# Kernel optimization log

Hardware: AMD Instinct MI355X
Metric: run time of the kernel (lower is better)

The kernel has to match this reference:

```python
import jax, jax.numpy as jnp
import numpy as np
import math

HEADS = 8
HID = 32
MODES = 8
IN_CH = 4
SEQ = 32
B = 2
H = 64
W = 64


def spectral_conv(x, wr, wi):
    # x: [N, Cin, H, W]; w: [Cin, Cout, m, m] complex (low rfft2 modes only)
    n, _, h, w = x.shape
    m = wr.shape[2]
    xf = jnp.fft.rfft2(x)  # [N, Cin, H, W//2+1] complex64
    of = jnp.einsum('bixy,ioxy->boxy', xf[:, :, :m, :m], wr + 1j * wi)
    out_ft = jnp.zeros((n, wr.shape[1], h, w // 2 + 1), dtype=of.dtype)
    out_ft = out_ft.at[:, :, :m, :m].set(of)
    return jnp.fft.irfft2(out_ft, s=(h, w))


def conv1x1(x, w, b):
    # x: [N, Cin, H, W], w: [Cout, Cin], b: [Cout]
    return jnp.einsum('bchw,oc->bohw', x, w) + b[None, :, None, None]


def setup_inputs() -> dict:
    key = jax.random.key(0)
    ks = jax.random.split(key, 16)
    hd = HEADS * HID
    s = 0.02
    inp = {
        'v': jax.random.normal(ks[0], (B, SEQ, IN_CH, H, W), dtype=jnp.float32),
        'qwr': jax.random.normal(ks[1], (IN_CH, hd, MODES, MODES), dtype=jnp.float32) * s,
        'qwi': jax.random.normal(ks[2], (IN_CH, hd, MODES, MODES), dtype=jnp.float32) * s,
        'kwr': jax.random.normal(ks[3], (IN_CH, hd, MODES, MODES), dtype=jnp.float32) * s,
        'kwi': jax.random.normal(ks[4], (IN_CH, hd, MODES, MODES), dtype=jnp.float32) * s,
        'vwr': jax.random.normal(ks[5], (IN_CH, hd, MODES, MODES), dtype=jnp.float32) * s,
        'vwi': jax.random.normal(ks[6], (IN_CH, hd, MODES, MODES), dtype=jnp.float32) * s,
        'u1wr': jax.random.normal(ks[7], (hd, HID, MODES, MODES), dtype=jnp.float32) * s,
        'u1wi': jax.random.normal(ks[8], (hd, HID, MODES, MODES), dtype=jnp.float32) * s,
        'u2wr': jax.random.normal(ks[9], (HID, IN_CH, MODES, MODES), dtype=jnp.float32) * s,
        'u2wi': jax.random.normal(ks[10], (HID, IN_CH, MODES, MODES), dtype=jnp.float32) * s,
        's1w': jax.random.normal(ks[11], (HID, hd), dtype=jnp.float32) * s,
        's1b': jnp.zeros((HID,), dtype=jnp.float32),
        's2w': jax.random.normal(ks[12], (IN_CH, HID), dtype=jnp.float32) * s,
        's2b': jnp.zeros((IN_CH,), dtype=jnp.float32),
    }
    return inp


def reference(v, qwr, qwi, kwr, kwi, vwr, vwi, u1wr, u1wi, u2wr, u2wi, s1w, s1b, s2w, s2b):
    b, s, c, h, w = v.shape
    scale = 1.0 / math.sqrt(HID / HEADS)
    vr = v.reshape(b * s, c, h, w)
    embed = (b, HEADS, s, -1, h, w)  # same raw row-major reshape as torch
    q = spectral_conv(vr, qwr, qwi).reshape(embed)
    k = spectral_conv(vr, kwr, kwi).reshape(embed)
    val = spectral_conv(vr, vwr, vwi).reshape(embed)
    # inner products over channel dim, then dx^2-weighted spatial integral
    ip = jnp.einsum('bhsdrc,bhtdrc->bhstrc', q, k) * scale
    dx = 1.0 / h
    l2 = jnp.sum(ip, axis=(-2, -1)) * (dx * dx)  # [b, h, s1, s2]
    A = jax.nn.softmax(l2, axis=-1)
    u = jnp.einsum('bhst,bhtdrc->bhsdrc', A, val)
    u = jnp.transpose(u, (0, 2, 1, 3, 4, 5)).reshape(b * s, HEADS * u.shape[3], h, w)
    # SimpleFNO: gelu(conv1) + skip1, then conv2 + skip2
    x1 = jax.nn.gelu(spectral_conv(u, u1wr, u1wi), approximate=False) + conv1x1(u, s1w, s1b)
    x2 = spectral_conv(x1, u2wr, u2wi) + conv1x1(x1, s2w, s2b)
    return x2.reshape(b, s, c, h, w)
```

## Files before the change

kernel.cpp:

```cpp
#include <hip/hip_runtime.h>
#include <math.h>

#define HEADS 8
#define HIDC  32
#define MODES 8
#define IN_CH 4
#define SEQ   32
#define NS    64
#define HD    256
#define NM    64
#define NPIX  4096
#define TWO_PI_D 6.283185307179586476925286766559

__device__ __forceinline__ float2 f2(float a, float b){ return make_float2(a,b); }

__global__ __launch_bounds__(256) void fwd_dft_kernel(const float* __restrict__ src,
                                                      float2* __restrict__ dst){
  int f = blockIdx.x;
  const float* fld = src + (size_t)f * NPIX;
  __shared__ float  s_fld[64*65];
  __shared__ float2 s_cs[64];
  __shared__ float2 s_a1[64][8];
  int tid = threadIdx.x;
  for (int k = tid; k < NPIX; k += 256) s_fld[(k>>6)*65 + (k&63)] = fld[k];
  if (tid < 64){ double sv, cv; sincos(TWO_PI_D * tid / 64.0, &sv, &cv); s_cs[tid] = f2((float)cv,(float)sv); }
  __syncthreads();
  for (int o = tid; o < 512; o += 256){
    int y = o >> 3, kx = o & 7;
    const float* row = s_fld + y*65;
    float sr = 0.f, si = 0.f;
    for (int x = 0; x < 64; ++x){
      float2 cs = s_cs[(kx*x) & 63];
      float v = row[x];
      sr += v * cs.x; si -= v * cs.y;
    }
    s_a1[y][kx] = f2(sr, si);
  }
  __syncthreads();
  if (tid < 64){
    int ky = tid >> 3, kx = tid & 7;
    float sr = 0.f, si = 0.f;
    for (int y = 0; y < 64; ++y){
      float2 a = s_a1[y][kx];
      float2 cs = s_cs[(ky*y) & 63];
      sr += a.x*cs.x + a.y*cs.y;
      si += a.y*cs.x - a.x*cs.y;
    }
    dst[(size_t)f*NM + tid] = f2(sr, si);
  }
}

__global__ __launch_bounds__(256) void gram_kernel(const float* __restrict__ qwr, const float* __restrict__ qwi,
                                                   const float* __restrict__ kwr, const float* __restrict__ kwi,
                                                   float2* __restrict__ G2, float* __restrict__ Gdc){
  int m = blockIdx.x, tid = threadIdx.x;
  __shared__ float qsr[4][257], qsi[4][257], ksr[4][257], ksi[4][257];
  for (int k = tid; k < 1024; k += 256){
    int i = k >> 8, c = k & 255;
    size_t a = ((size_t)(i*256 + c))*64 + m;
    qsr[i][c] = qwr[a]; qsi[i][c] = qwi[a];
    ksr[i][c] = kwr[a]; ksi[i][c] = kwi[a];
  }
  __syncthreads();
  int kx = m & 7, ky = m >> 3;
  float w = (kx >= 1) ? 2.0f : ((ky >= 1) ? 0.5f : 0.0f);
  for (int e = tid; e < 1024; e += 256){
    int P = e >> 7, T = (e >> 4) & 7, i = (e >> 2) & 3, j = e & 3;
    float grr=0.f, gri=0.f, gir=0.f, gii=0.f;
    for (int d = 0; d < 32; ++d){
      float ar = qsr[i][P*32+d], ai = qsi[i][P*32+d];
      float br = ksr[j][T*32+d], bi = ksi[j][T*32+d];
      grr += ar*br; gri += ar*bi; gir += ai*br; gii += ai*bi;
    }
    G2[(size_t)(((m*8+P)*4+i)*4+j)*8 + T] = f2(w*(grr+gii), w*(gir-gri));
    if (m == 0){
      int o = ((P*4+i)*4+j)*8 + T;
      Gdc[o] = grr; Gdc[1024+o] = gri; Gdc[2048+o] = gir; Gdc[3072+o] = gii;
    }
  }
}

__global__ __launch_bounds__(256) void attn_kernel(const float2* __restrict__ Vf,
                                                   const float2* __restrict__ G2,
                                                   const float* __restrict__ Gdc,
                                                   float* __restrict__ A){
  int bx = blockIdx.x;
  int s = bx & 31;
  int base = ((bx >> 8) * 32) + (((bx >> 5) & 7) * 4);
  int tid = threadIdx.x;
  int t = tid & 31, mc = tid >> 5;
  __shared__ float2 s_vf[4][IN_CH][64];
  __shared__ float  s_part[8][33];
  for (int k = tid; k < 4*IN_CH*64; k += 256){
    int m = k & 63, c = (k>>6)&3, smp = k>>8;
    s_vf[smp][c][m] = Vf[((size_t)(base+smp)*IN_CH + c)*NM + m];
  }
  __syncthreads();
  int sg = s >> 3, P = s & 7;
  int tg = t >> 3, T = t & 7;
  float acc = 0.f;
  for (int mm = 0; mm < 8; ++mm){
    int m = mc*8 + mm;
    const float2* g = G2 + (size_t)((m*8+P)*16)*8 + T;
    float sub = 0.f;
    for (int i = 0; i < 4; ++i){
      float2 a = s_vf[sg][i][m];
      for (int j = 0; j < 4; ++j){
        float2 b = s_vf[tg][j][m];
        float zr = a.x*b.x + a.y*b.y;
        float zi = a.y*b.x - a.x*b.y;
        float2 gv = g[(size_t)(i*4+j)*8];
        sub += zr*gv.x - zi*gv.y;
      }
    }
    acc += sub;
  }
  if (mc == 0){
    float sub = 0.f;
    for (int i = 0; i < 4; ++i){
      float2 a = s_vf[sg][i][0];
      for (int j = 0; j < 4; ++j){
        float2 b = s_vf[tg][j][0];
        int o = ((P*4+i)*4+j)*8 + T;
        sub += a.x*b.x*Gdc[o] - a.x*b.y*Gdc[1024+o]
             - a.y*b.x*Gdc[2048+o] + a.y*b.y*Gdc[3072+o];
      }
    }
    acc += sub;
  }
  s_part[mc][t] = acc;
  __syncthreads();
  if (tid < 32){
    float l2 = 0.f;
    for (int k = 0; k < 8; ++k) l2 += s_part[k][tid];
    l2 *= 0.5f / (4096.0f * 4096.0f);
    float mx = l2;
    for (int off = 16; off; off >>= 1) mx = fmaxf(mx, __shfl_xor(mx, off, 32));
    float e = expf(l2 - mx);
    float sm = e;
    for (int off = 16; off; off >>= 1) sm += __shfl_xor(sm, off, 32);
    A[(size_t)bx*32 + tid] = e / sm;
  }
}

__global__ __launch_bounds__(256) void uspec_kernel(const float2* __restrict__ Vf,
                                                    const float* __restrict__ vwr, const float* __restrict__ vwi,
                                                    const float* __restrict__ A,
                                                    float2* __restrict__ Uf){
  int bid = blockIdx.x;
  int b = bid >> 7, hh = (bid >> 4) & 7, mq = bid & 15, m0 = mq*4;
  int nbase = b*32 + hh*4;
  int tid = threadIdx.x;
  __shared__ float2 s_vw[4][4][256];
  __shared__ float2 s_vv[4][4][256];
  __shared__ float  s_A[32][32];
  __shared__ float2 s_vf[4][4][4];
  for (int k = tid; k < 4096; k += 256){
    int i = k >> 10, c = (k >> 2) & 255, mm = k & 3;
    size_t a = ((size_t)(i*256 + c))*64 + m0 + mm;
    s_vw[i][mm][c] = f2(vwr[a], vwi[a]);
  }
  for (int k = tid; k < 1024; k += 256)
    s_A[k>>5][k&31] = A[(size_t)((b*8+hh)*32 + (k>>5))*32 + (k&31)];
  if (tid < 64){
    int smp = tid >> 4, i = (tid >> 2) & 3, mm = tid & 3;
    s_vf[smp][i][mm] = Vf[((size_t)(nbase+smp)*4 + i)*64 + m0 + mm];
  }
  __syncthreads();
  for (int k = tid; k < 4096; k += 256){
    int smp = k >> 10, mm = (k >> 8) & 3, c = k & 255;
    float sr = 0.f, si = 0.f;
    for (int i = 0; i < 4; ++i){
      float2 v = s_vf[smp][i][mm];
      float2 w = s_vw[i][mm][c];
      sr += v.x*w.x - v.y*w.y;
      si += v.x*w.y + v.y*w.x;
    }
    s_vv[smp][mm][c] = f2(sr, si);
  }
  __syncthreads();
  int sg = tid >> 5, d = tid & 31;
  float2 acc[4][4];
  for (int ss = 0; ss < 4; ++ss)
    for (int mm = 0; mm < 4; ++mm) acc[ss][mm] = f2(0.f, 0.f);
  for (int tt = 0; tt < 32; ++tt){
    int tg = tt >> 3, c = (tt & 7)*32 + d;
    float a0 = s_A[sg*4+0][tt], a1 = s_A[sg*4+1][tt];
    float a2 = s_A[sg*4+2][tt], a3 = s_A[sg*4+3][tt];
    for (int mm = 0; mm < 4; ++mm){
      float2 v = s_vv[tg][mm][c];
      acc[0][mm].x += a0*v.x; acc[0][mm].y += a0*v.y;
      acc[1][mm].x += a1*v.x; acc[1][mm].y += a1*v.y;
      acc[2][mm].x += a2*v.x; acc[2][mm].y += a2*v.y;
      acc[3][mm].x += a3*v.x; acc[3][mm].y += a3*v.y;
    }
  }
  for (int ss = 0; ss < 4; ++ss){
    int n = b*32 + sg*4 + ss;
    for (int mm = 0; mm < 4; ++mm)
      Uf[((size_t)n*64 + m0 + mm)*256 + hh*32 + d] = acc[ss][mm];
  }
}

__global__ __launch_bounds__(256) void mix1_kernel(const float2* __restrict__ Uf,
                                                   const float* __restrict__ u1wr, const float* __restrict__ u1wi,
                                                   const float* __restrict__ s1w,
                                                   float2* __restrict__ U1f, float2* __restrict__ S1f){
  int n = blockIdx.x >> 2, mq = blockIdx.x & 3, m0 = mq*16;
  int tid = threadIdx.x;
  __shared__ float2 s_u[16][258];
  __shared__ float  s_w1[32][257];
  for (int k = tid; k < 16*256; k += 256){
    int c = k & 255, mm = k >> 8;
    s_u[mm][c] = Uf[((size_t)n*64 + m0 + mm)*256 + c];
  }
  for (int k = tid; k < 32*256; k += 256){
    int c = k & 255, o1 = k >> 8;
    s_w1[o1][c] = s1w[o1*256 + c];
  }
  __syncthreads();
  int o1 = tid >> 3, m8 = tid & 7;
  int mA = m0 + m8, mB = m0 + m8 + 8;
  float prA = ((mA & 7)==0 && mA) ? 0.5f : 1.0f;  float piA = mA ? prA : 0.0f;
  float prB = ((mB & 7)==0 && mB) ? 0.5f : 1.0f;  float piB = mB ? prB : 0.0f;
  float2 au0 = f2(0,0), au1 = f2(0,0), as0 = f2(0,0), as1 = f2(0,0);
  for (int c = 0; c < 256; ++c){
    float2 uA = s_u[m8][c], uB = s_u[m8+8][c];
    float sw = s_w1[o1][c];
    size_t wb = ((size_t)c*32 + o1)*64;
    float wrA = u1wr[wb + mA], wiA = u1wi[wb + mA];
    float wrB = u1wr[wb + mB], wiB = u1wi[wb + mB];
    float xA = uA.x*prA, yA = uA.y*piA;
    float xB = uB.x*prB, yB = uB.y*piB;
    au0.x += xA*wrA - yA*wiA;  au0.y += xA*wiA + yA*wrA;
    au1.x += xB*wrB - yB*wiB;  au1.y += xB*wiB + yB*wrB;
    as0.x += uA.x*sw; as0.y += uA.y*sw;
    as1.x += uB.x*sw; as1.y += uB.y*sw;
  }
  size_t ob = (size_t)(n*32 + o1)*64;
  U1f[ob + mA] = au0; U1f[ob + mB] = au1;
  S1f[ob + mA] = as0; S1f[ob + mB] = as1;
}

__global__ __launch_bounds__(256) void x1dft_kernel(const float2* __restrict__ U1f,
                                                    const float2* __restrict__ S1f,
                                                    const float* __restrict__ s1b,
                                                    float* __restrict__ x1,
                                                    float2* __restrict__ X1f){
  int f = blockIdx.x, o1 = f & 31, tid = threadIdx.x;
  __shared__ float2 s_cs[64];
  __shared__ float2 s_gu[64], s_gs[64];
  __shared__ float2 s_tu[64][8], s_ts[64][8];
  __shared__ float  s_fld[64*65];
  __shared__ float2 s_a1[64][8];
  if (tid < 64){ double sv, cv; sincos(TWO_PI_D*tid/64.0, &sv, &cv); s_cs[tid] = f2((float)cv,(float)sv); }
  else if (tid < 128) s_gu[tid-64]  = U1f[(size_t)f*NM + tid-64];
  else if (tid < 192) s_gs[tid-128] = S1f[(size_t)f*NM + tid-128];
  __syncthreads();
  for (int o = tid; o < 512; o += 256){
    int y = o >> 3, kx = o & 7;
    float wf = (kx ? 2.0f : 1.0f) * (1.0f/4096.0f);
    float ar=0.f, ai=0.f, br=0.f, bi=0.f;
    for (int ky = 0; ky < 8; ++ky){
      float2 cs = s_cs[(ky*y) & 63];
      float2 gu = s_gu[ky*8+kx], gs = s_gs[ky*8+kx];
      ar += gu.x*cs.x - gu.y*cs.y;  ai += gu.x*cs.y + gu.y*cs.x;
      br += gs.x*cs.x - gs.y*cs.y;  bi += gs.x*cs.y + gs.y*cs.x;
    }
    s_tu[y][kx] = f2(ar*wf, ai*wf);
    s_ts[y][kx] = f2(br*wf, bi*wf);
  }
  __syncthreads();
  float bias = s1b[o1];
  float* dst = x1 + (size_t)f*NPIX;
  for (int p = tid; p < NPIX; p += 256){
    int y = p >> 6, x = p & 63;
    float vu = 0.f, vs = 0.f;
    for (int kx = 0; kx < 8; ++kx){
      float2 cs = s_cs[(kx*x) & 63];
      float2 tu = s_tu[y][kx], ts = s_ts[y][kx];
      vu += tu.x*cs.x - tu.y*cs.y;
      vs += ts.x*cs.x - ts.y*cs.y;
    }
    float g = 0.5f * vu * (1.0f + erff(vu * 0.70710678f));
    float val = g + vs + bias;
    dst[p] = val;
    s_fld[y*65 + x] = val;
  }
  __syncthreads();
  for (int o = tid; o < 512; o += 256){
    int y = o >> 3, kx = o & 7;
    const float* row = s_fld + y*65;
    float sr = 0.f, si = 0.f;
    for (int x = 0; x < 64; ++x){
      float2 cs = s_cs[(kx*x) & 63];
      float v = row[x];
      sr += v*cs.x; si -= v*cs.y;
    }
    s_a1[y][kx] = f2(sr, si);
  }
  __syncthreads();
  if (tid < 64){
    int ky = tid >> 3, kx = tid & 7;
    float sr = 0.f, si = 0.f;
    for (int y = 0; y < 64; ++y){
      float2 a = s_a1[y][kx];
      float2 cs = s_cs[(ky*y) & 63];
      sr += a.x*cs.x + a.y*cs.y;
      si += a.y*cs.x - a.x*cs.y;
    }
    X1f[(size_t)f*NM + tid] = f2(sr, si);
  }
}

__global__ __launch_bounds__(256) void final_kernel(const float2* __restrict__ X1f,
                                                    const float* __restrict__ u2wr, const float* __restrict__ u2wi,
                                                    const float* __restrict__ x1,
                                                    const float* __restrict__ s2w, const float* __restrict__ s2b,
                                                    float* __restrict__ out){
  int n = blockIdx.x >> 3, tile = blockIdx.x & 7;
  int tid = threadIdx.x;
  __shared__ float2 s_cs[64];
  __shared__ float2 s_x2f[4][64];
  __shared__ float2 s_tmp[4][64][8];
  __shared__ float  s_w2[128];
  __shared__ float  s_b2[4];
  if (tid < 64){ double sv, cv; sincos(TWO_PI_D*tid/64.0, &sv, &cv); s_cs[tid] = f2((float)cv,(float)sv); }
  if (tid >= 64 && tid < 192) s_w2[tid-64] = s2w[tid-64];
  if (tid >= 192 && tid < 196) s_b2[tid-192] = s2b[tid-192];
  {
    int o2 = tid >> 6, m = tid & 63;
    float sr = 0.f, si = 0.f;
    for (int o1 = 0; o1 < 32; ++o1){
      float2 xv = X1f[((size_t)n*HIDC + o1)*NM + m];
      size_t wb = ((size_t)(o1*IN_CH + o2))*NM + m;
      float wr = u2wr[wb], wi = u2wi[wb];
      sr += xv.x*wr - xv.y*wi;
      si += xv.x*wi + xv.y*wr;
    }
    s_x2f[o2][m] = f2(sr, si);
  }
  __syncthreads();
  for (int o = tid; o < 2048; o += 256){
    int o2 = o >> 9, rem = o & 511, y = rem >> 3, kx = rem & 7;
    float wf = (kx ? 2.0f : 1.0f) * (1.0f/4096.0f);
    float tr=0.f, ti=0.f;
    for (int ky = 0; ky < 8; ++ky){
      float2 cs = s_cs[(ky*y) & 63];
      float2 g = s_x2f[o2][ky*8+kx];
      tr += g.x*cs.x - g.y*cs.y;
      ti += g.x*cs.y + g.y*cs.x;
    }
    s_tmp[o2][y][kx] = f2(tr*wf, ti*wf);
  }
  __syncthreads();
  const float* xbase = x1 + (size_t)n*HIDC*NPIX;
  float* obase = out + (size_t)n*IN_CH*NPIX;
  for (int p = tile*512 + tid; p < (tile+1)*512; p += 256){
    float a0 = s_b2[0], a1 = s_b2[1], a2 = s_b2[2], a3 = s_b2[3];
    for (int c = 0; c < 32; ++c){
      float xv = xbase[(size_t)c*NPIX + p];
      a0 += s_w2[c]*xv; a1 += s_w2[32+c]*xv; a2 += s_w2[64+c]*xv; a3 += s_w2[96+c]*xv;
    }
    int y = p >> 6, x = p & 63;
    float sp[4];
    #pragma unroll
    for (int o2 = 0; o2 < 4; ++o2){
      float v = 0.f;
      for (int kx = 0; kx < 8; ++kx){
        float2 cs = s_cs[(kx*x) & 63];
        float2 t2 = s_tmp[o2][y][kx];
        v += t2.x*cs.x - t2.y*cs.y;
      }
      sp[o2] = v;
    }
    obase[p]          = a0 + sp[0];
    obase[NPIX + p]   = a1 + sp[1];
    obase[2*NPIX + p] = a2 + sp[2];
    obase[3*NPIX + p] = a3 + sp[3];
  }
}

extern "C" void kernel_launch(void* const* d_in, const int* in_sizes, int n_in,
                              void* d_out, int out_size, void* d_ws, size_t ws_size,
                              hipStream_t stream) {
  (void)in_sizes; (void)n_in; (void)out_size; (void)ws_size;
  const float* v    = (const float*)d_in[0];
  const float* qwr  = (const float*)d_in[1];
  const float* qwi  = (const float*)d_in[2];
  const float* kwr  = (const float*)d_in[3];
  const float* kwi  = (const float*)d_in[4];
  const float* vwr  = (const float*)d_in[5];
  const float* vwi  = (const float*)d_in[6];
  const float* u1wr = (const float*)d_in[7];
  const float* u1wi = (const float*)d_in[8];
  const float* u2wr = (const float*)d_in[9];
  const float* u2wi = (const float*)d_in[10];
  const float* s1w  = (const float*)d_in[11];
  const float* s1b  = (const float*)d_in[12];
  const float* s2w  = (const float*)d_in[13];
  const float* s2b  = (const float*)d_in[14];
  float* out = (float*)d_out;

  float* ws = (float*)d_ws;
  size_t off = 0;
  float2* Vf   = (float2*)(ws + off); off += (size_t)NS*IN_CH*NM*2;
  float2* G2   = (float2*)(ws + off); off += (size_t)65536*2;
  float*  Gdc  =          (ws + off); off += 4096;
  float*  A    =          (ws + off); off += 16384;
  float2* Uf   = (float2*)(ws + off); off += (size_t)NS*NM*HD*2;
  float2* U1f  = (float2*)(ws + off); off += (size_t)NS*HIDC*NM*2;
  float2* S1f  = (float2*)(ws + off); off += (size_t)NS*HIDC*NM*2;
  float*  x1   =          (ws + off); off += (size_t)NS*HIDC*NPIX;
  float2* X1f  = (float2*)(ws + off); off += (size_t)NS*HIDC*NM*2;

  fwd_dft_kernel<<<NS*IN_CH, 256, 0, stream>>>(v, Vf);
  gram_kernel<<<64, 256, 0, stream>>>(qwr, qwi, kwr, kwi, G2, Gdc);
  attn_kernel<<<512, 256, 0, stream>>>(Vf, G2, Gdc, A);
  uspec_kernel<<<256, 256, 0, stream>>>(Vf, vwr, vwi, A, Uf);
  mix1_kernel<<<256, 256, 0, stream>>>(Uf, u1wr, u1wi, s1w, U1f, S1f);
  x1dft_kernel<<<NS*HIDC, 256, 0, stream>>>(U1f, S1f, s1b, x1, X1f);
  final_kernel<<<64*8, 256, 0, stream>>>(X1f, u2wr, u2wi, x1, s2w, s2b, out);
}
```

Measured before the change: 224.0 us.

## Pre-transpose u1 weights, split uspec/mix1/final finer, tabulate DFT twiddles

Adds a kernel that transposes and pre-scales the u1 spectral weights into a float4 layout, so mix1 can read them coalesced with one thread per output and mode. uspec, mix1 and final are split into more, smaller blocks to raise parallelism. x1dft and final use a precomputed 64x8 twiddle table with float4 shared-memory reads and register-cached column twiddles in place of indexed cos/sin lookups. The transposed weights are stored in the x1 buffer, which x1dft overwrites later. The cost is an extra launch and redundant per-block work such as repeated twiddle and weight setup.

```diff
diff --git a/kernel.cpp b/kernel.cpp
--- a/kernel.cpp
+++ b/kernel.cpp
@@ -148,27 +148,28 @@
                                                     const float* __restrict__ A,
                                                     float2* __restrict__ Uf){
   int bid = blockIdx.x;
-  int b = bid >> 7, hh = (bid >> 4) & 7, mq = bid & 15, m0 = mq*4;
+  int mg = bid & 31, hh = (bid >> 5) & 7, b = bid >> 8;
+  int m0 = mg*2;
   int nbase = b*32 + hh*4;
   int tid = threadIdx.x;
-  __shared__ float2 s_vw[4][4][256];
-  __shared__ float2 s_vv[4][4][256];
-  __shared__ float  s_A[32][32];
-  __shared__ float2 s_vf[4][4][4];
-  for (int k = tid; k < 4096; k += 256){
-    int i = k >> 10, c = (k >> 2) & 255, mm = k & 3;
-    size_t a = ((size_t)(i*256 + c))*64 + m0 + mm;
+  __shared__ float2 s_vw[4][2][256];
+  __shared__ float2 s_vv[4][2][256];
+  __shared__ float  s_A[32][33];
+  __shared__ float2 s_vf[4][4][2];
+  for (int k = tid; k < 2048; k += 256){
+    int i = k >> 9, mm = (k >> 8) & 1, c = k & 255;
+    size_t a = ((size_t)i*256 + c)*64 + m0 + mm;
     s_vw[i][mm][c] = f2(vwr[a], vwi[a]);
   }
   for (int k = tid; k < 1024; k += 256)
     s_A[k>>5][k&31] = A[(size_t)((b*8+hh)*32 + (k>>5))*32 + (k&31)];
-  if (tid < 64){
-    int smp = tid >> 4, i = (tid >> 2) & 3, mm = tid & 3;
+  if (tid < 32){
+    int smp = tid >> 3, i = (tid >> 1) & 3, mm = tid & 1;
     s_vf[smp][i][mm] = Vf[((size_t)(nbase+smp)*4 + i)*64 + m0 + mm];
   }
   __syncthreads();
-  for (int k = tid; k < 4096; k += 256){
-    int smp = k >> 10, mm = (k >> 8) & 3, c = k & 255;
+  for (int k = tid; k < 2048; k += 256){
+    int smp = k >> 9, mm = (k >> 8) & 1, c = k & 255;
     float sr = 0.f, si = 0.f;
     for (int i = 0; i < 4; ++i){
       float2 v = s_vf[smp][i][mm];
@@ -180,14 +181,14 @@
   }
   __syncthreads();
   int sg = tid >> 5, d = tid & 31;
-  float2 acc[4][4];
+  float2 acc[4][2];
   for (int ss = 0; ss < 4; ++ss)
-    for (int mm = 0; mm < 4; ++mm) acc[ss][mm] = f2(0.f, 0.f);
+    for (int mm = 0; mm < 2; ++mm) acc[ss][mm] = f2(0.f, 0.f);
   for (int tt = 0; tt < 32; ++tt){
     int tg = tt >> 3, c = (tt & 7)*32 + d;
     float a0 = s_A[sg*4+0][tt], a1 = s_A[sg*4+1][tt];
     float a2 = s_A[sg*4+2][tt], a3 = s_A[sg*4+3][tt];
-    for (int mm = 0; mm < 4; ++mm){
+    for (int mm = 0; mm < 2; ++mm){
       float2 v = s_vv[tg][mm][c];
       acc[0][mm].x += a0*v.x; acc[0][mm].y += a0*v.y;
       acc[1][mm].x += a1*v.x; acc[1][mm].y += a1*v.y;
@@ -197,49 +198,52 @@
   }
   for (int ss = 0; ss < 4; ++ss){
     int n = b*32 + sg*4 + ss;
-    for (int mm = 0; mm < 4; ++mm)
+    for (int mm = 0; mm < 2; ++mm)
       Uf[((size_t)n*64 + m0 + mm)*256 + hh*32 + d] = acc[ss][mm];
   }
 }
 
-__global__ __launch_bounds__(256) void mix1_kernel(const float2* __restrict__ Uf,
-                                                   const float* __restrict__ u1wr, const float* __restrict__ u1wi,
+__global__ __launch_bounds__(256) void u1t_kernel(const float* __restrict__ u1wr,
+                                                  const float* __restrict__ u1wi,
+                                                  float4* __restrict__ u1wT){
+  int t = blockIdx.x*256 + threadIdx.x;
+  int o1 = t & 31, c = (t>>5) & 255, m = t >> 13;
+  float pr = ((m & 7)==0 && m) ? 0.5f : 1.0f;
+  float pi = m ? pr : 0.0f;
+  size_t src = ((size_t)c*32 + o1)*64 + m;
+  float wr = u1wr[src], wi = u1wi[src];
+  u1wT[t] = make_float4(pr*wr, pi*wi, pr*wi, pi*wr);
+}
+
+__global__ __launch_bounds__(128) void mix1_kernel(const float2* __restrict__ Uf,
+                                                   const float4* __restrict__ u1wT,
                                                    const float* __restrict__ s1w,
                                                    float2* __restrict__ U1f, float2* __restrict__ S1f){
-  int n = blockIdx.x >> 2, mq = blockIdx.x & 3, m0 = mq*16;
+  int n = blockIdx.x >> 4, mg = blockIdx.x & 15, m0 = mg*4;
   int tid = threadIdx.x;
-  __shared__ float2 s_u[16][258];
-  __shared__ float  s_w1[32][257];
-  for (int k = tid; k < 16*256; k += 256){
-    int c = k & 255, mm = k >> 8;
+  __shared__ float2 s_u[4][256];
+  for (int k = tid; k < 1024; k += 128){
+    int mm = k >> 8, c = k & 255;
     s_u[mm][c] = Uf[((size_t)n*64 + m0 + mm)*256 + c];
   }
-  for (int k = tid; k < 32*256; k += 256){
-    int c = k & 255, o1 = k >> 8;
-    s_w1[o1][c] = s1w[o1*256 + c];
-  }
-  __syncthreads();
-  int o1 = tid >> 3, m8 = tid & 7;
-  int mA = m0 + m8, mB = m0 + m8 + 8;
-  float prA = ((mA & 7)==0 && mA) ? 0.5f : 1.0f;  float piA = mA ? prA : 0.0f;
-  float prB = ((mB & 7)==0 && mB) ? 0.5f : 1.0f;  float piB = mB ? prB : 0.0f;
-  float2 au0 = f2(0,0), au1 = f2(0,0), as0 = f2(0,0), as1 = f2(0,0);
+  __syncthreads();
+  int o1 = tid & 31, mm = tid >> 5;
+  int m = m0 + mm;
+  const float4* wp = u1wT + (size_t)m*256*32 + o1;
+  const float* swp = s1w + o1*256;
+  float2 au = f2(0.f,0.f), asv = f2(0.f,0.f);
+  #pragma unroll 8
   for (int c = 0; c < 256; ++c){
-    float2 uA = s_u[m8][c], uB = s_u[m8+8][c];
-    float sw = s_w1[o1][c];
-    size_t wb = ((size_t)c*32 + o1)*64;
-    float wrA = u1wr[wb + mA], wiA = u1wi[wb + mA];
-    float wrB = u1wr[wb + mB], wiB = u1wi[wb + mB];
-    float xA = uA.x*prA, yA = uA.y*piA;
-    float xB = uB.x*prB, yB = uB.y*piB;
-    au0.x += xA*wrA - yA*wiA;  au0.y += xA*wiA + yA*wrA;
-    au1.x += xB*wrB - yB*wiB;  au1.y += xB*wiB + yB*wrB;
-    as0.x += uA.x*sw; as0.y += uA.y*sw;
-    as1.x += uB.x*sw; as1.y += uB.y*sw;
-  }
-  size_t ob = (size_t)(n*32 + o1)*64;
-  U1f[ob + mA] = au0; U1f[ob + mB] = au1;
-  S1f[ob + mA] = as0; S1f[ob + mB] = as1;
+    float2 u = s_u[mm][c];
+    float4 w = wp[(size_t)c*32];
+    float sw = swp[c];
+    au.x  += u.x*w.x - u.y*w.y;
+    au.y  += u.x*w.z + u.y*w.w;
+    asv.x += u.x*sw;
+    asv.y += u.y*sw;
+  }
+  size_t ob = ((size_t)n*32 + o1)*64 + m;
+  U1f[ob] = au; S1f[ob] = asv;
 }
 
 __global__ __launch_bounds__(256) void x1dft_kernel(const float2* __restrict__ U1f,
@@ -248,21 +252,25 @@
                                                     float* __restrict__ x1,
                                                     float2* __restrict__ X1f){
   int f = blockIdx.x, o1 = f & 31, tid = threadIdx.x;
-  __shared__ float2 s_cs[64];
+  __shared__ float2 s_e[64][8];
   __shared__ float2 s_gu[64], s_gs[64];
   __shared__ float2 s_tu[64][8], s_ts[64][8];
-  __shared__ float  s_fld[64*65];
+  __shared__ float  s_fld[64*68];
   __shared__ float2 s_a1[64][8];
-  if (tid < 64){ double sv, cv; sincos(TWO_PI_D*tid/64.0, &sv, &cv); s_cs[tid] = f2((float)cv,(float)sv); }
-  else if (tid < 128) s_gu[tid-64]  = U1f[(size_t)f*NM + tid-64];
-  else if (tid < 192) s_gs[tid-128] = S1f[(size_t)f*NM + tid-128];
+  for (int e = tid; e < 512; e += 256){
+    int a = e >> 3, b = e & 7;
+    double sv, cv; sincos(TWO_PI_D * ((a*b) & 63) / 64.0, &sv, &cv);
+    s_e[a][b] = f2((float)cv, (float)sv);
+  }
+  if (tid >= 128 && tid < 192) s_gu[tid-128] = U1f[(size_t)f*NM + tid-128];
+  else if (tid >= 192) s_gs[tid-192] = S1f[(size_t)f*NM + tid-192];
   __syncthreads();
   for (int o = tid; o < 512; o += 256){
     int y = o >> 3, kx = o & 7;
     float wf = (kx ? 2.0f : 1.0f) * (1.0f/4096.0f);
     float ar=0.f, ai=0.f, br=0.f, bi=0.f;
     for (int ky = 0; ky < 8; ++ky){
-      float2 cs = s_cs[(ky*y) & 63];
+      float2 cs = s_e[y][ky];
       float2 gu = s_gu[ky*8+kx], gs = s_gs[ky*8+kx];
       ar += gu.x*cs.x - gu.y*cs.y;  ai += gu.x*cs.y + gu.y*cs.x;
       br += gs.x*cs.x - gs.y*cs.y;  bi += gs.x*cs.y + gs.y*cs.x;
@@ -271,31 +279,50 @@
     s_ts[y][kx] = f2(br*wf, bi*wf);
   }
   __syncthreads();
+  int xx = tid & 63;
+  float2 ce[8];
+  {
+    const float4* ep = (const float4*)&s_e[xx][0];
+    float4 e0 = ep[0], e1 = ep[1], e2 = ep[2], e3 = ep[3];
+    ce[0]=f2(e0.x,e0.y); ce[1]=f2(e0.z,e0.w);
+    ce[2]=f2(e1.x,e1.y); ce[3]=f2(e1.z,e1.w);
+    ce[4]=f2(e2.x,e2.y); ce[5]=f2(e2.z,e2.w);
+    ce[6]=f2(e3.x,e3.y); ce[7]=f2(e3.z,e3.w);
+  }
   float bias = s1b[o1];
   float* dst = x1 + (size_t)f*NPIX;
-  for (int p = tid; p < NPIX; p += 256){
-    int y = p >> 6, x = p & 63;
-    float vu = 0.f, vs = 0.f;
-    for (int kx = 0; kx < 8; ++kx){
-      float2 cs = s_cs[(kx*x) & 63];
-      float2 tu = s_tu[y][kx], ts = s_ts[y][kx];
-      vu += tu.x*cs.x - tu.y*cs.y;
-      vs += ts.x*cs.x - ts.y*cs.y;
-    }
+  for (int i = 0; i < 16; ++i){
+    int p = i*256 + tid;
+    int y = p >> 6;
+    const float4* tp = (const float4*)&s_tu[y][0];
+    float4 t0 = tp[0], t1 = tp[1], t2 = tp[2], t3 = tp[3];
+    const float4* up = (const float4*)&s_ts[y][0];
+    float4 u0 = up[0], u1 = up[1], u2 = up[2], u3 = up[3];
+    float vu = t0.x*ce[0].x - t0.y*ce[0].y + t0.z*ce[1].x - t0.w*ce[1].y
+             + t1.x*ce[2].x - t1.y*ce[2].y + t1.z*ce[3].x - t1.w*ce[3].y
+             + t2.x*ce[4].x - t2.y*ce[4].y + t2.z*ce[5].x - t2.w*ce[5].y
+             + t3.x*ce[6].x - t3.y*ce[6].y + t3.z*ce[7].x - t3.w*ce[7].y;
+    float vs = u0.x*ce[0].x - u0.y*ce[0].y + u0.z*ce[1].x - u0.w*ce[1].y
+             + u1.x*ce[2].x - u1.y*ce[2].y + u1.z*ce[3].x - u1.w*ce[3].y
+             + u2.x*ce[4].x - u2.y*ce[4].y + u2.z*ce[5].x - u2.w*ce[5].y
+             + u3.x*ce[6].x - u3.y*ce[6].y + u3.z*ce[7].x - u3.w*ce[7].y;
     float g = 0.5f * vu * (1.0f + erff(vu * 0.70710678f));
     float val = g + vs + bias;
     dst[p] = val;
-    s_fld[y*65 + x] = val;
+    s_fld[y*68 + xx] = val;
   }
   __syncthreads();
   for (int o = tid; o < 512; o += 256){
     int y = o >> 3, kx = o & 7;
-    const float* row = s_fld + y*65;
-    float sr = 0.f, si = 0.f;
-    for (int x = 0; x < 64; ++x){
-      float2 cs = s_cs[(kx*x) & 63];
-      float v = row[x];
-      sr += v*cs.x; si -= v*cs.y;
+    const float4* row = (const float4*)&s_fld[y*68];
+    float sr = 0.f, si = 0.f;
+    for (int x4 = 0; x4 < 16; ++x4){
+      float4 v = row[x4];
+      int xb = x4*4;
+      float2 c0 = s_e[xb+0][kx], c1 = s_e[xb+1][kx];
+      float2 c2 = s_e[xb+2][kx], c3 = s_e[xb+3][kx];
+      sr += v.x*c0.x + v.y*c1.x + v.z*c2.x + v.w*c3.x;
+      si -= v.x*c0.y + v.y*c1.y + v.z*c2.y + v.w*c3.y;
     }
     s_a1[y][kx] = f2(sr, si);
   }
@@ -305,7 +332,7 @@
     float sr = 0.f, si = 0.f;
     for (int y = 0; y < 64; ++y){
       float2 a = s_a1[y][kx];
-      float2 cs = s_cs[(ky*y) & 63];
+      float2 cs = s_e[y][ky];
       sr += a.x*cs.x + a.y*cs.y;
       si += a.y*cs.x - a.x*cs.y;
     }
@@ -318,16 +345,20 @@
                                                     const float* __restrict__ x1,
                                                     const float* __restrict__ s2w, const float* __restrict__ s2b,
                                                     float* __restrict__ out){
-  int n = blockIdx.x >> 3, tile = blockIdx.x & 7;
+  int n = blockIdx.x >> 4, tile = blockIdx.x & 15;
   int tid = threadIdx.x;
-  __shared__ float2 s_cs[64];
+  __shared__ float2 s_e[64][8];
   __shared__ float2 s_x2f[4][64];
   __shared__ float2 s_tmp[4][64][8];
   __shared__ float  s_w2[128];
   __shared__ float  s_b2[4];
-  if (tid < 64){ double sv, cv; sincos(TWO_PI_D*tid/64.0, &sv, &cv); s_cs[tid] = f2((float)cv,(float)sv); }
-  if (tid >= 64 && tid < 192) s_w2[tid-64] = s2w[tid-64];
-  if (tid >= 192 && tid < 196) s_b2[tid-192] = s2b[tid-192];
+  for (int e = tid; e < 512; e += 256){
+    int a = e >> 3, b = e & 7;
+    double sv, cv; sincos(TWO_PI_D * ((a*b) & 63) / 64.0, &sv, &cv);
+    s_e[a][b] = f2((float)cv, (float)sv);
+  }
+  if (tid < 128) s_w2[tid] = s2w[tid];
+  if (tid >= 128 && tid < 132) s_b2[tid-128] = s2b[tid-128];
   {
     int o2 = tid >> 6, m = tid & 63;
     float sr = 0.f, si = 0.f;
@@ -346,7 +377,7 @@
     float wf = (kx ? 2.0f : 1.0f) * (1.0f/4096.0f);
     float tr=0.f, ti=0.f;
     for (int ky = 0; ky < 8; ++ky){
-      float2 cs = s_cs[(ky*y) & 63];
+      float2 cs = s_e[y][ky];
       float2 g = s_x2f[o2][ky*8+kx];
       tr += g.x*cs.x - g.y*cs.y;
       ti += g.x*cs.y + g.y*cs.x;
@@ -354,31 +385,39 @@
     s_tmp[o2][y][kx] = f2(tr*wf, ti*wf);
   }
   __syncthreads();
+  int p = tile*256 + tid;
+  int y = p >> 6, xx = p & 63;
+  float2 ce[8];
+  {
+    const float4* ep = (const float4*)&s_e[xx][0];
+    float4 e0 = ep[0], e1 = ep[1], e2 = ep[2], e3 = ep[3];
+    ce[0]=f2(e0.x,e0.y); ce[1]=f2(e0.z,e0.w);
+    ce[2]=f2(e1.x,e1.y); ce[3]=f2(e1.z,e1.w);
+    ce[4]=f2(e2.x,e2.y); ce[5]=f2(e2.z,e2.w);
+    ce[6]=f2(e3.x,e3.y); ce[7]=f2(e3.z,e3.w);
+  }
   const float* xbase = x1 + (size_t)n*HIDC*NPIX;
   float* obase = out + (size_t)n*IN_CH*NPIX;
-  for (int p = tile*512 + tid; p < (tile+1)*512; p += 256){
-    float a0 = s_b2[0], a1 = s_b2[1], a2 = s_b2[2], a3 = s_b2[3];
-    for (int c = 0; c < 32; ++c){
-      float xv = xbase[(size_t)c*NPIX + p];
-      a0 += s_w2[c]*xv; a1 += s_w2[32+c]*xv; a2 += s_w2[64+c]*xv; a3 += s_w2[96+c]*xv;
-    }
-    int y = p >> 6, x = p & 63;
-    float sp[4];
-    #pragma unroll
-    for (int o2 = 0; o2 < 4; ++o2){
-      float v = 0.f;
-      for (int kx = 0; kx < 8; ++kx){
-        float2 cs = s_cs[(kx*x) & 63];
-        float2 t2 = s_tmp[o2][y][kx];
-        v += t2.x*cs.x - t2.y*cs.y;
-      }
-      sp[o2] = v;
-    }
-    obase[p]          = a0 + sp[0];
-    obase[NPIX + p]   = a1 + sp[1];
-    obase[2*NPIX + p] = a2 + sp[2];
-    obase[3*NPIX + p] = a3 + sp[3];
-  }
+  float a0 = s_b2[0], a1 = s_b2[1], a2 = s_b2[2], a3 = s_b2[3];
+  #pragma unroll 8
+  for (int c = 0; c < 32; ++c){
+    float xv = xbase[(size_t)c*NPIX + p];
+    a0 += s_w2[c]*xv; a1 += s_w2[32+c]*xv; a2 += s_w2[64+c]*xv; a3 += s_w2[96+c]*xv;
+  }
+  float sp[4];
+  #pragma unroll
+  for (int o2 = 0; o2 < 4; ++o2){
+    const float4* tp = (const float4*)&s_tmp[o2][y][0];
+    float4 t0 = tp[0], t1 = tp[1], t2 = tp[2], t3 = tp[3];
+    sp[o2] = t0.x*ce[0].x - t0.y*ce[0].y + t0.z*ce[1].x - t0.w*ce[1].y
+           + t1.x*ce[2].x - t1.y*ce[2].y + t1.z*ce[3].x - t1.w*ce[3].y
+           + t2.x*ce[4].x - t2.y*ce[4].y + t2.z*ce[5].x - t2.w*ce[5].y
+           + t3.x*ce[6].x - t3.y*ce[6].y + t3.z*ce[7].x - t3.w*ce[7].y;
+  }
+  obase[p]          = a0 + sp[0];
+  obase[NPIX + p]   = a1 + sp[1];
+  obase[2*NPIX + p] = a2 + sp[2];
+  obase[3*NPIX + p] = a3 + sp[3];
 }
 
 extern "C" void kernel_launch(void* const* d_in, const int* in_sizes, int n_in,
@@ -413,12 +452,14 @@
   float2* S1f  = (float2*)(ws + off); off += (size_t)NS*HIDC*NM*2;
   float*  x1   =          (ws + off); off += (size_t)NS*HIDC*NPIX;
   float2* X1f  = (float2*)(ws + off); off += (size_t)NS*HIDC*NM*2;
+  float4* u1wT = (float4*)x1;
 
   fwd_dft_kernel<<<NS*IN_CH, 256, 0, stream>>>(v, Vf);
   gram_kernel<<<64, 256, 0, stream>>>(qwr, qwi, kwr, kwi, G2, Gdc);
+  u1t_kernel<<<2048, 256, 0, stream>>>(u1wr, u1wi, u1wT);
   attn_kernel<<<512, 256, 0, stream>>>(Vf, G2, Gdc, A);
-  uspec_kernel<<<256, 256, 0, stream>>>(Vf, vwr, vwi, A, Uf);
-  mix1_kernel<<<256, 256, 0, stream>>>(Uf, u1wr, u1wi, s1w, U1f, S1f);
+  uspec_kernel<<<512, 256, 0, stream>>>(Vf, vwr, vwi, A, Uf);
+  mix1_kernel<<<1024, 128, 0, stream>>>(Uf, u1wT, s1w, U1f, S1f);
   x1dft_kernel<<<NS*HIDC, 256, 0, stream>>>(U1f, S1f, s1b, x1, X1f);
-  final_kernel<<<64*8, 256, 0, stream>>>(X1f, u2wr, u2wi, x1, s2w, s2b, out);
-}
+  final_kernel<<<64*16, 256, 0, stream>>>(X1f, u2wr, u2wi, x1, s2w, s2b, out);
+}
```

After: 227.2 us. About the same (+1.4%).
